# Performance work log

Measured on AMD Instinct MI355X. Metric: run time of the kernel, lower is better.

## Reference

```python
import jax, jax.numpy as jnp
import numpy as np

B, S, K, H = 512, 200, 16, 256
EPS_LN = 1e-12
EPS_COS = 1e-6


def layernorm(x, w, b):
    u = x.mean(-1, keepdims=True)
    s = ((x - u) ** 2).mean(-1, keepdims=True)
    return w * (x - u) / jnp.sqrt(s + EPS_LN) + b


def setup_inputs() -> dict:
    key = jax.random.key(0)
    ks = jax.random.split(key, 10)
    inv_sqrt_h = 1.0 / np.sqrt(H)
    inp = {
        "z": jax.random.normal(ks[0], (B, S, H), dtype=jnp.float32),
        "prototypes": jax.random.normal(ks[1], (K, H), dtype=jnp.float32) * inv_sqrt_h,
        "ln1_w": jnp.ones((H,), jnp.float32), "ln1_b": jnp.zeros((H,), jnp.float32),
        "ln2_w": jnp.ones((H,), jnp.float32), "ln2_b": jnp.zeros((H,), jnp.float32),
        "ln3_w": jnp.ones((H,), jnp.float32), "ln3_b": jnp.zeros((H,), jnp.float32),
        "ln4_w": jnp.ones((H,), jnp.float32), "ln4_b": jnp.zeros((H,), jnp.float32),
        "ln5_w": jnp.ones((H,), jnp.float32), "ln5_b": jnp.zeros((H,), jnp.float32),
        "w_weight": jax.random.normal(ks[2], (H, H), dtype=jnp.float32) * inv_sqrt_h,
        "w_bias": jax.random.normal(ks[3], (H,), dtype=jnp.float32) * 0.02,
        "b_prime": jax.random.normal(ks[4], (H,), dtype=jnp.float32) * 0.02,
        "alphas": jax.random.normal(ks[5], (S, H), dtype=jnp.float32) * 0.02,
        "beta_input_seq": jax.random.normal(ks[6], (K, H), dtype=jnp.float32) * inv_sqrt_h,
        "beta_label_seq": jax.random.normal(ks[7], (K, H), dtype=jnp.float32) * inv_sqrt_h,
        "is_input_seq": 1,
    }
    return inp


def reference(z, prototypes, ln1_w, ln1_b, ln2_w, ln2_b, ln3_w, ln3_b,
              ln4_w, ln4_b, ln5_w, ln5_b, w_weight, w_bias, b_prime,
              alphas, beta_input_seq, beta_label_seq, is_input_seq):
    inv_sqrt_h = 1.0 / np.sqrt(z.shape[-1])

    # ---- intention clustering: cosine-sim of z against each prototype, softmax over K ----
    zn = layernorm(z, ln1_w, ln1_b)                      # [B,S,H]
    pn = layernorm(prototypes, ln2_w, ln2_b)             # [K,H]
    z_norm = jnp.maximum(jnp.linalg.norm(zn, axis=-1), EPS_COS)   # [B,S]
    p_norm = jnp.maximum(jnp.linalg.norm(pn, axis=-1), EPS_COS)   # [K]
    cos = jnp.einsum('bsh,kh->bsk', zn, pn) / (z_norm[..., None] * p_norm[None, None, :])
    p_k_i = jax.nn.softmax(cos * inv_sqrt_h, axis=-1)    # [B,S,K]

    # ---- intention weighting: key transform + bmm attention over positions ----
    keys_tilde = layernorm(z + alphas, ln3_w, ln3_b)                         # [B,S,H]
    keys = keys_tilde + jax.nn.relu(keys_tilde @ w_weight.T + w_bias)        # [B,S,H]
    query = layernorm(b_prime + alphas[-1, :] + z[:, -1, :], ln4_w, ln4_b)   # [B,H]
    scores = jnp.einsum('bsh,bh->bs', keys, query)                           # [B,S]
    p_i = jax.nn.softmax(scores * inv_sqrt_h, axis=-1)                       # [B,S]

    # ---- aggregation ----
    attn = p_k_i * p_i[..., None]                        # [B,S,K]
    beta = beta_input_seq if is_input_seq else beta_label_seq
    enc = beta + jnp.einsum('bsk,bsh->bkh', attn, z)     # [B,K,H]
    return layernorm(enc, ln5_w, ln5_b)
```

## Files before the change

kernel.cpp:

```cpp
#include <hip/hip_runtime.h>
#include <hip/hip_bf16.h>

#define NB 512
#define NS 200
#define NK 16
#define NH 256
#define INV_SQRT_H 0.0625f
#define EPS_LN 1e-12f
#define EPS_COS 1e-6f
#define KTPAD 264

typedef __attribute__((ext_vector_type(8))) short bf16x8;
typedef __attribute__((ext_vector_type(4))) short s16x4;
typedef __attribute__((ext_vector_type(4))) float f32x4;

__device__ __forceinline__ float wred_sum(float v) {
    v += __shfl_xor(v, 1);  v += __shfl_xor(v, 2);  v += __shfl_xor(v, 4);
    v += __shfl_xor(v, 8);  v += __shfl_xor(v, 16); v += __shfl_xor(v, 32);
    return v;
}

__device__ __forceinline__ float red16(float v) {
    v += __shfl_xor(v, 1);  v += __shfl_xor(v, 2);
    v += __shfl_xor(v, 4);  v += __shfl_xor(v, 8);
    return v;
}

__device__ __forceinline__ float red32(float v) {
    v += __shfl_xor(v, 1);  v += __shfl_xor(v, 2);  v += __shfl_xor(v, 4);
    v += __shfl_xor(v, 8);  v += __shfl_xor(v, 16);
    return v;
}

__device__ __forceinline__ float block_sum256(float v, float* scr) {
    v = wred_sum(v);
    int w = threadIdx.x >> 6;
    __syncthreads();
    if ((threadIdx.x & 63) == 0) scr[w] = v;
    __syncthreads();
    return scr[0] + scr[1] + scr[2] + scr[3];
}

__global__ __launch_bounds__(256) void k_prep(
        const float* __restrict__ prot, const float* __restrict__ w2, const float* __restrict__ b2,
        const float* __restrict__ w_weight, __hip_bfloat16* __restrict__ w_bf,
        const float* __restrict__ z, const float* __restrict__ b_prime,
        const float* __restrict__ alphas, const float* __restrict__ w4, const float* __restrict__ b4,
        float* __restrict__ pn_div, float* __restrict__ q) {
    __shared__ float scr[4];
    int t = threadIdx.x;
    int bid = blockIdx.x;
    if (bid == 0) {
        int c = t & 15, k = t >> 4;
        int h0 = c * 4;
        f32x4 x[4];
        float sm = 0.f, sq = 0.f;
#pragma unroll
        for (int j = 0; j < 4; ++j) {
            x[j] = *reinterpret_cast<const f32x4*>(prot + k * NH + h0 + 64 * j);
#pragma unroll
            for (int i = 0; i < 4; ++i) { sm += x[j][i]; sq += x[j][i] * x[j][i]; }
        }
        sm = red16(sm); sq = red16(sq);
        float u = sm * (1.f / NH);
        float var = sq * (1.f / NH) - u * u;
        float rstd = rsqrtf(var + EPS_LN);
        f32x4 pn[4];
        float nsq = 0.f;
#pragma unroll
        for (int j = 0; j < 4; ++j) {
            f32x4 wv = *reinterpret_cast<const f32x4*>(w2 + h0 + 64 * j);
            f32x4 bv = *reinterpret_cast<const f32x4*>(b2 + h0 + 64 * j);
#pragma unroll
            for (int i = 0; i < 4; ++i) {
                pn[j][i] = wv[i] * (x[j][i] - u) * rstd + bv[i];
                nsq += pn[j][i] * pn[j][i];
            }
        }
        nsq = red16(nsq);
        float pinv = 1.f / fmaxf(sqrtf(nsq), EPS_COS);
#pragma unroll
        for (int j = 0; j < 4; ++j) {
            f32x4 o = pn[j] * pinv;
            *reinterpret_cast<f32x4*>(pn_div + k * NH + h0 + 64 * j) = o;
        }
    } else if (bid <= 64) {
        int i = ((bid - 1) * 256 + t) * 4;
        f32x4 w = *reinterpret_cast<const f32x4*>(w_weight + i);
        union { s16x4 v; __hip_bfloat16 h[4]; } u;
#pragma unroll
        for (int j = 0; j < 4; ++j) u.h[j] = __float2bfloat16(w[j]);
        *reinterpret_cast<s16x4*>(w_bf + i) = u.v;
    } else {
        int b = bid - 65;
        float x = b_prime[t] + alphas[(NS - 1) * NH + t] + z[((size_t)b * NS + (NS - 1)) * NH + t];
        float u = block_sum256(x, scr) * (1.f / NH);
        float d = x - u;
        float var = block_sum256(d * d, scr) * (1.f / NH);
        q[b * NH + t] = w4[t] * d * rsqrtf(var + EPS_LN) + b4[t];
    }
}

__global__ __launch_bounds__(256) void k_rows(
        const float* __restrict__ z, const float* __restrict__ pn_div,
        const float* __restrict__ ln1w, const float* __restrict__ ln1b,
        const float* __restrict__ ln3w, const float* __restrict__ ln3b,
        const float* __restrict__ alphas, const float* __restrict__ q,
        float* __restrict__ p_k_i, __hip_bfloat16* __restrict__ kt,
        float* __restrict__ scores) {
    int tid = threadIdx.x;
    int c   = tid & 31;
    int row = blockIdx.x * 8 + (tid >> 5);
    int s   = row % NS;
    int b   = row / NS;
    size_t base = (size_t)row * NH;
    int h0 = c * 8;

    f32x4 zv0 = *reinterpret_cast<const f32x4*>(z + base + h0);
    f32x4 zv1 = *reinterpret_cast<const f32x4*>(z + base + h0 + 4);
    float sm = 0.f, sq = 0.f;
#pragma unroll
    for (int i = 0; i < 4; ++i) { sm += zv0[i] + zv1[i]; sq += zv0[i]*zv0[i] + zv1[i]*zv1[i]; }
    sm = red32(sm); sq = red32(sq);
    float u    = sm * (1.f / NH);
    float var  = sq * (1.f / NH) - u * u;
    float rstd = rsqrtf(var + EPS_LN);

    f32x4 zn0, zn1;
    {
        f32x4 w1a = *reinterpret_cast<const f32x4*>(ln1w + h0);
        f32x4 w1b = *reinterpret_cast<const f32x4*>(ln1w + h0 + 4);
        f32x4 b1a = *reinterpret_cast<const f32x4*>(ln1b + h0);
        f32x4 b1b = *reinterpret_cast<const f32x4*>(ln1b + h0 + 4);
        float nsq = 0.f;
#pragma unroll
        for (int i = 0; i < 4; ++i) {
            zn0[i] = w1a[i] * (zv0[i] - u) * rstd + b1a[i];
            zn1[i] = w1b[i] * (zv1[i] - u) * rstd + b1b[i];
            nsq += zn0[i]*zn0[i] + zn1[i]*zn1[i];
        }
        nsq = red32(nsq);
        float inv_zn = 1.f / fmaxf(sqrtf(nsq), EPS_COS);
        sm = inv_zn;
    }
    float inv_zn = sm;

    float acc[NK];
#pragma unroll
    for (int k = 0; k < NK; ++k) {
        f32x4 pa = *reinterpret_cast<const f32x4*>(pn_div + k * NH + h0);
        f32x4 pb = *reinterpret_cast<const f32x4*>(pn_div + k * NH + h0 + 4);
        acc[k] = zn0[0]*pa[0] + zn0[1]*pa[1] + zn0[2]*pa[2] + zn0[3]*pa[3]
               + zn1[0]*pb[0] + zn1[1]*pb[1] + zn1[2]*pb[2] + zn1[3]*pb[3];
    }
#pragma unroll
    for (int r = 0; r < 4; ++r) {
        int m = 1 << r;
        int n = NK >> r;
        bool hi = (c & m) != 0;
#pragma unroll
        for (int i = 0; i < 8; ++i) {
            if (i < n / 2) {
                float a = acc[2 * i], bb = acc[2 * i + 1];
                float x = hi ? a : bb;
                float y = __shfl_xor(x, m);
                acc[i] = (hi ? bb : a) + y;
            }
        }
    }
    acc[0] += __shfl_xor(acc[0], 16);

    float logit = acc[0] * inv_zn * INV_SQRT_H;
    float mx = logit;
    mx = fmaxf(mx, __shfl_xor(mx, 1)); mx = fmaxf(mx, __shfl_xor(mx, 2));
    mx = fmaxf(mx, __shfl_xor(mx, 4)); mx = fmaxf(mx, __shfl_xor(mx, 8));
    float e = __expf(logit - mx);
    float se = e;
    se += __shfl_xor(se, 1); se += __shfl_xor(se, 2);
    se += __shfl_xor(se, 4); se += __shfl_xor(se, 8);
    if (c < NK) p_k_i[(size_t)row * NK + c] = e / se;

    f32x4 xv0, xv1;
    {
        f32x4 za = *reinterpret_cast<const f32x4*>(z + base + h0);
        f32x4 zb = *reinterpret_cast<const f32x4*>(z + base + h0 + 4);
        f32x4 aa = *reinterpret_cast<const f32x4*>(alphas + s * NH + h0);
        f32x4 ab = *reinterpret_cast<const f32x4*>(alphas + s * NH + h0 + 4);
        xv0 = za + aa; xv1 = zb + ab;
    }
    float sm3 = 0.f, sq3 = 0.f;
#pragma unroll
    for (int i = 0; i < 4; ++i) { sm3 += xv0[i] + xv1[i]; sq3 += xv0[i]*xv0[i] + xv1[i]*xv1[i]; }
    sm3 = red32(sm3); sq3 = red32(sq3);
    float u3 = sm3 * (1.f / NH);
    float v3 = sq3 * (1.f / NH) - u3 * u3;
    float r3 = rsqrtf(v3 + EPS_LN);

    float ktq = 0.f;
    union { bf16x8 v; __hip_bfloat16 h[8]; } kv;
    {
        f32x4 w3a = *reinterpret_cast<const f32x4*>(ln3w + h0);
        f32x4 w3b = *reinterpret_cast<const f32x4*>(ln3w + h0 + 4);
        f32x4 b3a = *reinterpret_cast<const f32x4*>(ln3b + h0);
        f32x4 b3b = *reinterpret_cast<const f32x4*>(ln3b + h0 + 4);
        f32x4 qa  = *reinterpret_cast<const f32x4*>(q + b * NH + h0);
        f32x4 qb  = *reinterpret_cast<const f32x4*>(q + b * NH + h0 + 4);
#pragma unroll
        for (int i = 0; i < 4; ++i) {
            float k0 = w3a[i] * (xv0[i] - u3) * r3 + b3a[i];
            float k1 = w3b[i] * (xv1[i] - u3) * r3 + b3b[i];
            kv.h[i]     = __float2bfloat16(k0);
            kv.h[i + 4] = __float2bfloat16(k1);
            ktq += k0 * qa[i] + k1 * qb[i];
        }
    }
    *reinterpret_cast<bf16x8*>(kt + base + h0) = kv.v;
    ktq = red32(ktq);
    if (c == 0) scores[row] = ktq;
}

__global__ __launch_bounds__(256) void k_gemm_scores(
        const __hip_bfloat16* __restrict__ kt, const __hip_bfloat16* __restrict__ w_bf,
        const float* __restrict__ w_bias, const float* __restrict__ q,
        float* __restrict__ scores) {
    __shared__ __hip_bfloat16 kt_lds[64 * KTPAD];
    __shared__ float sc[4][64];
    int tid = threadIdx.x, wave = tid >> 6, lane = tid & 63;
    int g = lane >> 4, cc = lane & 15;
    int row0 = blockIdx.x * 64;
    int n_base = wave * 64;

#pragma unroll
    for (int u = 0; u < 8; ++u) {
        int ci = u * 256 + tid;
        bf16x8 v = *reinterpret_cast<const bf16x8*>(kt + (size_t)row0 * NH + ci * 8);
        int r = ci >> 5;
        int col = (ci & 31) * 8;
        *reinterpret_cast<bf16x8*>(&kt_lds[r * KTPAD + col]) = v;
    }
    __syncthreads();

    f32x4 acc[4][4];
#pragma unroll
    for (int mf = 0; mf < 4; ++mf)
#pragma unroll
        for (int nf = 0; nf < 4; ++nf) { f32x4 zz = {0.f, 0.f, 0.f, 0.f}; acc[mf][nf] = zz; }

#pragma unroll
    for (int ks = 0; ks < 8; ++ks) {
        bf16x8 a[4], bb[4];
#pragma unroll
        for (int mf = 0; mf < 4; ++mf)
            a[mf] = *reinterpret_cast<const bf16x8*>(&kt_lds[(mf * 16 + cc) * KTPAD + ks * 32 + g * 8]);
#pragma unroll
        for (int nf = 0; nf < 4; ++nf)
            bb[nf] = *reinterpret_cast<const bf16x8*>(
                w_bf + (size_t)(n_base + nf * 16 + cc) * NH + ks * 32 + g * 8);
#pragma unroll
        for (int mf = 0; mf < 4; ++mf)
#pragma unroll
            for (int nf = 0; nf < 4; ++nf)
                acc[mf][nf] = __builtin_amdgcn_mfma_f32_16x16x32_bf16(a[mf], bb[nf], acc[mf][nf], 0, 0, 0);
    }

    int b_lo = row0 / NS, b_hi = (row0 + 63) / NS;
    float q_lo[4], q_hi[4];
#pragma unroll
    for (int nf = 0; nf < 4; ++nf) {
        int n = n_base + nf * 16 + cc;
        q_lo[nf] = q[b_lo * NH + n];
        q_hi[nf] = q[b_hi * NH + n];
    }

#pragma unroll
    for (int mf = 0; mf < 4; ++mf) {
#pragma unroll
        for (int r = 0; r < 4; ++r) {
            int m = mf * 16 + g * 4 + r;
            int row = row0 + m;
            bool hi = (row / NS) != b_lo;
            float partial = 0.f;
#pragma unroll
            for (int nf = 0; nf < 4; ++nf) {
                int n = n_base + nf * 16 + cc;
                float uval = acc[mf][nf][r] + w_bias[n];
                partial += fmaxf(uval, 0.f) * (hi ? q_hi[nf] : q_lo[nf]);
            }
            partial += __shfl_xor(partial, 1, 16);
            partial += __shfl_xor(partial, 2, 16);
            partial += __shfl_xor(partial, 4, 16);
            partial += __shfl_xor(partial, 8, 16);
            if (cc == 0) sc[wave][m] = partial;
        }
    }
    __syncthreads();
    if (tid < 64)
        scores[row0 + tid] += sc[0][tid] + sc[1][tid] + sc[2][tid] + sc[3][tid];
}

__global__ __launch_bounds__(512) void k_final(
        const float* __restrict__ z, const float* __restrict__ scores,
        const float* __restrict__ p_k_i,
        const float* __restrict__ beta_in, const float* __restrict__ beta_lb,
        const int* __restrict__ flag,
        const float* __restrict__ ln5w, const float* __restrict__ ln5b,
        float* __restrict__ out) {
    __shared__ float p_i[NS];
    __shared__ f32x4 attn4[NS * 4];
    __shared__ f32x4 encp[NK][64];
    int tid = threadIdx.x, lane = tid & 63, wave = tid >> 6;
    int b = blockIdx.x;

    if (wave == 0) {
        float l[4]; float mx = -1e30f;
#pragma unroll
        for (int j = 0; j < 4; ++j) {
            int s = lane + 64 * j;
            l[j] = (s < NS) ? scores[b * NS + s] * INV_SQRT_H : -1e30f;
            mx = fmaxf(mx, l[j]);
        }
#pragma unroll
        for (int m = 1; m < 64; m <<= 1) mx = fmaxf(mx, __shfl_xor(mx, m));
        float ev[4]; float se = 0.f;
#pragma unroll
        for (int j = 0; j < 4; ++j) {
            int s = lane + 64 * j;
            ev[j] = (s < NS) ? __expf(l[j] - mx) : 0.f;
            se += ev[j];
        }
        se = wred_sum(se);
        float inv = 1.f / se;
#pragma unroll
        for (int j = 0; j < 4; ++j) {
            int s = lane + 64 * j;
            if (s < NS) p_i[s] = ev[j] * inv;
        }
    }
    __syncthreads();
    for (int idx = tid; idx < NS * 4; idx += 512) {
        f32x4 pk = *reinterpret_cast<const f32x4*>(p_k_i + (size_t)b * NS * NK + idx * 4);
        attn4[idx] = pk * p_i[idx >> 2];
    }
    __syncthreads();

    const float* beta = (*flag) ? beta_in : beta_lb;
    int kg = wave & 3;
    int sh = wave >> 2;
    int k0 = kg * 4;
    int h0 = lane * 4;
    f32x4 acc[4];
#pragma unroll
    for (int kk = 0; kk < 4; ++kk) {
        if (sh == 0)
            acc[kk] = *reinterpret_cast<const f32x4*>(beta + (k0 + kk) * NH + h0);
        else
            { f32x4 zz = {0.f,0.f,0.f,0.f}; acc[kk] = zz; }
    }

    const float* zb = z + (size_t)b * NS * NH + h0;
    int s0 = sh * 100;
    for (int s = s0; s < s0 + 100; s += 4) {
        f32x4 zv0 = *reinterpret_cast<const f32x4*>(zb + (s + 0) * NH);
        f32x4 zv1 = *reinterpret_cast<const f32x4*>(zb + (s + 1) * NH);
        f32x4 zv2 = *reinterpret_cast<const f32x4*>(zb + (s + 2) * NH);
        f32x4 zv3 = *reinterpret_cast<const f32x4*>(zb + (s + 3) * NH);
        f32x4 at0 = attn4[(s + 0) * 4 + kg];
        f32x4 at1 = attn4[(s + 1) * 4 + kg];
        f32x4 at2 = attn4[(s + 2) * 4 + kg];
        f32x4 at3 = attn4[(s + 3) * 4 + kg];
#pragma unroll
        for (int kk = 0; kk < 4; ++kk)
            acc[kk] += at0[kk] * zv0 + at1[kk] * zv1 + at2[kk] * zv2 + at3[kk] * zv3;
    }

    if (sh == 1) {
#pragma unroll
        for (int kk = 0; kk < 4; ++kk) encp[k0 + kk][lane] = acc[kk];
    }
    __syncthreads();
    if (sh == 0) {
        f32x4 w5 = *reinterpret_cast<const f32x4*>(ln5w + h0);
        f32x4 b5 = *reinterpret_cast<const f32x4*>(ln5b + h0);
#pragma unroll
        for (int kk = 0; kk < 4; ++kk) {
            acc[kk] += encp[k0 + kk][lane];
            float sm = acc[kk][0] + acc[kk][1] + acc[kk][2] + acc[kk][3];
            float sq = acc[kk][0]*acc[kk][0] + acc[kk][1]*acc[kk][1]
                     + acc[kk][2]*acc[kk][2] + acc[kk][3]*acc[kk][3];
            sm = wred_sum(sm); sq = wred_sum(sq);
            float u = sm * (1.f / NH);
            float var = sq * (1.f / NH) - u * u;
            float rstd = rsqrtf(var + EPS_LN);
            f32x4 o;
#pragma unroll
            for (int j = 0; j < 4; ++j) o[j] = w5[j] * (acc[kk][j] - u) * rstd + b5[j];
            *reinterpret_cast<f32x4*>(out + ((size_t)b * NK + k0 + kk) * NH + h0) = o;
        }
    }
}

extern "C" void kernel_launch(void* const* d_in, const int* in_sizes, int n_in,
                              void* d_out, int out_size, void* d_ws, size_t ws_size,
                              hipStream_t stream) {
    const float* z        = (const float*)d_in[0];
    const float* prot     = (const float*)d_in[1];
    const float* ln1w     = (const float*)d_in[2];
    const float* ln1b     = (const float*)d_in[3];
    const float* ln2w     = (const float*)d_in[4];
    const float* ln2b     = (const float*)d_in[5];
    const float* ln3w     = (const float*)d_in[6];
    const float* ln3b     = (const float*)d_in[7];
    const float* ln4w     = (const float*)d_in[8];
    const float* ln4b     = (const float*)d_in[9];
    const float* ln5w     = (const float*)d_in[10];
    const float* ln5b     = (const float*)d_in[11];
    const float* w_weight = (const float*)d_in[12];
    const float* w_bias   = (const float*)d_in[13];
    const float* b_prime  = (const float*)d_in[14];
    const float* alphas   = (const float*)d_in[15];
    const float* beta_in  = (const float*)d_in[16];
    const float* beta_lb  = (const float*)d_in[17];
    const int*   flag     = (const int*)d_in[18];
    float* out = (float*)d_out;

    char* ws = (char*)d_ws;
    float*          pn_div = (float*)(ws);
    float*          q      = (float*)(ws + 16384);
    __hip_bfloat16* w_bf   = (__hip_bfloat16*)(ws + 540672);
    float*          p_k_i  = (float*)(ws + 671744);
    float*          scores = (float*)(ws + 7225344);
    __hip_bfloat16* kt     = (__hip_bfloat16*)(ws + 7634944);

    k_prep<<<577, 256, 0, stream>>>(prot, ln2w, ln2b, w_weight, w_bf,
                                    z, b_prime, alphas, ln4w, ln4b, pn_div, q);
    k_rows<<<NB * NS / 8, 256, 0, stream>>>(z, pn_div, ln1w, ln1b, ln3w, ln3b,
                                            alphas, q, p_k_i, kt, scores);
    k_gemm_scores<<<NB * NS / 64, 256, 0, stream>>>(kt, w_bf, w_bias, q, scores);
    k_final<<<NB, 512, 0, stream>>>(z, scores, p_k_i, beta_in, beta_lb, flag, ln5w, ln5b, out);
}
```

Before: 317.0 us.

## Compute cosine logits via bf16 MFMA on raw z with folded LayerNorm constants

The prototype projection is rewritten algebraically: LN1 weight is folded into bf16 prototypes, and per-prototype constants A and B are precomputed so logits become rstd*(z·p̃ - u*A) + B. Each block now handles 64 rows, stages bf16 z in LDS, runs a 16x16x32 MFMA for the z-by-prototype product, and does the softmax over K per row. This removes the per-row shuffle-transpose dot-product reduction. The scores epilogue in the GEMM kernel also replaces per-row shuffle reductions with an LDS transpose-sum. Rounding raw z to bf16 before subtracting the mean can lose precision when rows have a large mean.

```diff
diff --git a/kernel.cpp b/kernel.cpp
--- a/kernel.cpp
+++ b/kernel.cpp
@@ -43,10 +43,12 @@
 
 __global__ __launch_bounds__(256) void k_prep(
         const float* __restrict__ prot, const float* __restrict__ w2, const float* __restrict__ b2,
+        const float* __restrict__ ln1w, const float* __restrict__ ln1b,
         const float* __restrict__ w_weight, __hip_bfloat16* __restrict__ w_bf,
         const float* __restrict__ z, const float* __restrict__ b_prime,
         const float* __restrict__ alphas, const float* __restrict__ w4, const float* __restrict__ b4,
-        float* __restrict__ pn_div, float* __restrict__ q) {
+        __hip_bfloat16* __restrict__ ptil, float* __restrict__ Acst, float* __restrict__ Bcst,
+        float* __restrict__ q) {
     __shared__ float scr[4];
     int t = threadIdx.x;
     int bid = blockIdx.x;
@@ -79,11 +81,23 @@
         }
         nsq = red16(nsq);
         float pinv = 1.f / fmaxf(sqrtf(nsq), EPS_COS);
-#pragma unroll
-        for (int j = 0; j < 4; ++j) {
+        float asum = 0.f, bsum = 0.f;
+#pragma unroll
+        for (int j = 0; j < 4; ++j) {
+            f32x4 w1 = *reinterpret_cast<const f32x4*>(ln1w + h0 + 64 * j);
+            f32x4 b1 = *reinterpret_cast<const f32x4*>(ln1b + h0 + 64 * j);
             f32x4 o = pn[j] * pinv;
-            *reinterpret_cast<f32x4*>(pn_div + k * NH + h0 + 64 * j) = o;
-        }
+            union { s16x4 v; __hip_bfloat16 h[4]; } pt;
+#pragma unroll
+            for (int i = 0; i < 4; ++i) {
+                pt.h[i] = __float2bfloat16(w1[i] * o[i]);
+                asum += w1[i] * o[i];
+                bsum += b1[i] * o[i];
+            }
+            *reinterpret_cast<s16x4*>(ptil + k * NH + h0 + 64 * j) = pt.v;
+        }
+        asum = red16(asum); bsum = red16(bsum);
+        if (c == 0) { Acst[k] = asum; Bcst[k] = bsum; }
     } else if (bid <= 64) {
         int i = ((bid - 1) * 256 + t) * 4;
         f32x4 w = *reinterpret_cast<const f32x4*>(w_weight + i);
@@ -101,122 +115,147 @@
     }
 }
 
-__global__ __launch_bounds__(256) void k_rows(
-        const float* __restrict__ z, const float* __restrict__ pn_div,
+__global__ __launch_bounds__(256) void k_rows_mfma(
+        const float* __restrict__ z,
         const float* __restrict__ ln1w, const float* __restrict__ ln1b,
         const float* __restrict__ ln3w, const float* __restrict__ ln3b,
         const float* __restrict__ alphas, const float* __restrict__ q,
+        const __hip_bfloat16* __restrict__ ptil,
+        const float* __restrict__ Acst, const float* __restrict__ Bcst,
         float* __restrict__ p_k_i, __hip_bfloat16* __restrict__ kt,
         float* __restrict__ scores) {
+    __shared__ __hip_bfloat16 zbf[64 * KTPAD];
+    __shared__ float zp[64 * 17];
+    __shared__ float uu[64], rs[64], izn[64];
+    __shared__ float Al[16], Bl[16];
+
     int tid = threadIdx.x;
     int c   = tid & 31;
-    int row = blockIdx.x * 8 + (tid >> 5);
-    int s   = row % NS;
-    int b   = row / NS;
-    size_t base = (size_t)row * NH;
+    int grp = tid >> 5;
+    int row0 = blockIdx.x * 64;
     int h0 = c * 8;
 
-    f32x4 zv0 = *reinterpret_cast<const f32x4*>(z + base + h0);
-    f32x4 zv1 = *reinterpret_cast<const f32x4*>(z + base + h0 + 4);
-    float sm = 0.f, sq = 0.f;
-#pragma unroll
-    for (int i = 0; i < 4; ++i) { sm += zv0[i] + zv1[i]; sq += zv0[i]*zv0[i] + zv1[i]*zv1[i]; }
-    sm = red32(sm); sq = red32(sq);
-    float u    = sm * (1.f / NH);
-    float var  = sq * (1.f / NH) - u * u;
-    float rstd = rsqrtf(var + EPS_LN);
-
-    f32x4 zn0, zn1;
-    {
-        f32x4 w1a = *reinterpret_cast<const f32x4*>(ln1w + h0);
-        f32x4 w1b = *reinterpret_cast<const f32x4*>(ln1w + h0 + 4);
-        f32x4 b1a = *reinterpret_cast<const f32x4*>(ln1b + h0);
-        f32x4 b1b = *reinterpret_cast<const f32x4*>(ln1b + h0 + 4);
+    if (tid < 16) { Al[tid] = Acst[tid]; Bl[tid] = Bcst[tid]; }
+
+#pragma unroll 1
+    for (int jr = 0; jr < 8; ++jr) {
+        int rl  = grp + 8 * jr;
+        int row = row0 + rl;
+        int s   = row % NS;
+        int b   = row / NS;
+        size_t base = (size_t)row * NH;
+
+        f32x4 zv0 = *reinterpret_cast<const f32x4*>(z + base + h0);
+        f32x4 zv1 = *reinterpret_cast<const f32x4*>(z + base + h0 + 4);
+        float sm = 0.f, sq = 0.f;
+#pragma unroll
+        for (int i = 0; i < 4; ++i) { sm += zv0[i] + zv1[i]; sq += zv0[i]*zv0[i] + zv1[i]*zv1[i]; }
+        sm = red32(sm); sq = red32(sq);
+        float u    = sm * (1.f / NH);
+        float var  = sq * (1.f / NH) - u * u;
+        float rstd = rsqrtf(var + EPS_LN);
+
         float nsq = 0.f;
-#pragma unroll
-        for (int i = 0; i < 4; ++i) {
-            zn0[i] = w1a[i] * (zv0[i] - u) * rstd + b1a[i];
-            zn1[i] = w1b[i] * (zv1[i] - u) * rstd + b1b[i];
-            nsq += zn0[i]*zn0[i] + zn1[i]*zn1[i];
+        {
+            f32x4 w1a = *reinterpret_cast<const f32x4*>(ln1w + h0);
+            f32x4 w1b = *reinterpret_cast<const f32x4*>(ln1w + h0 + 4);
+            f32x4 b1a = *reinterpret_cast<const f32x4*>(ln1b + h0);
+            f32x4 b1b = *reinterpret_cast<const f32x4*>(ln1b + h0 + 4);
+#pragma unroll
+            for (int i = 0; i < 4; ++i) {
+                float a = w1a[i] * (zv0[i] - u) * rstd + b1a[i];
+                float d = w1b[i] * (zv1[i] - u) * rstd + b1b[i];
+                nsq += a * a + d * d;
+            }
         }
         nsq = red32(nsq);
-        float inv_zn = 1.f / fmaxf(sqrtf(nsq), EPS_COS);
-        sm = inv_zn;
-    }
-    float inv_zn = sm;
-
-    float acc[NK];
-#pragma unroll
-    for (int k = 0; k < NK; ++k) {
-        f32x4 pa = *reinterpret_cast<const f32x4*>(pn_div + k * NH + h0);
-        f32x4 pb = *reinterpret_cast<const f32x4*>(pn_div + k * NH + h0 + 4);
-        acc[k] = zn0[0]*pa[0] + zn0[1]*pa[1] + zn0[2]*pa[2] + zn0[3]*pa[3]
-               + zn1[0]*pb[0] + zn1[1]*pb[1] + zn1[2]*pb[2] + zn1[3]*pb[3];
-    }
-#pragma unroll
-    for (int r = 0; r < 4; ++r) {
-        int m = 1 << r;
-        int n = NK >> r;
-        bool hi = (c & m) != 0;
-#pragma unroll
-        for (int i = 0; i < 8; ++i) {
-            if (i < n / 2) {
-                float a = acc[2 * i], bb = acc[2 * i + 1];
-                float x = hi ? a : bb;
-                float y = __shfl_xor(x, m);
-                acc[i] = (hi ? bb : a) + y;
-            }
-        }
-    }
-    acc[0] += __shfl_xor(acc[0], 16);
-
-    float logit = acc[0] * inv_zn * INV_SQRT_H;
-    float mx = logit;
-    mx = fmaxf(mx, __shfl_xor(mx, 1)); mx = fmaxf(mx, __shfl_xor(mx, 2));
-    mx = fmaxf(mx, __shfl_xor(mx, 4)); mx = fmaxf(mx, __shfl_xor(mx, 8));
-    float e = __expf(logit - mx);
-    float se = e;
-    se += __shfl_xor(se, 1); se += __shfl_xor(se, 2);
-    se += __shfl_xor(se, 4); se += __shfl_xor(se, 8);
-    if (c < NK) p_k_i[(size_t)row * NK + c] = e / se;
-
-    f32x4 xv0, xv1;
-    {
-        f32x4 za = *reinterpret_cast<const f32x4*>(z + base + h0);
-        f32x4 zb = *reinterpret_cast<const f32x4*>(z + base + h0 + 4);
-        f32x4 aa = *reinterpret_cast<const f32x4*>(alphas + s * NH + h0);
-        f32x4 ab = *reinterpret_cast<const f32x4*>(alphas + s * NH + h0 + 4);
-        xv0 = za + aa; xv1 = zb + ab;
-    }
-    float sm3 = 0.f, sq3 = 0.f;
-#pragma unroll
-    for (int i = 0; i < 4; ++i) { sm3 += xv0[i] + xv1[i]; sq3 += xv0[i]*xv0[i] + xv1[i]*xv1[i]; }
-    sm3 = red32(sm3); sq3 = red32(sq3);
-    float u3 = sm3 * (1.f / NH);
-    float v3 = sq3 * (1.f / NH) - u3 * u3;
-    float r3 = rsqrtf(v3 + EPS_LN);
-
-    float ktq = 0.f;
-    union { bf16x8 v; __hip_bfloat16 h[8]; } kv;
-    {
-        f32x4 w3a = *reinterpret_cast<const f32x4*>(ln3w + h0);
-        f32x4 w3b = *reinterpret_cast<const f32x4*>(ln3w + h0 + 4);
-        f32x4 b3a = *reinterpret_cast<const f32x4*>(ln3b + h0);
-        f32x4 b3b = *reinterpret_cast<const f32x4*>(ln3b + h0 + 4);
-        f32x4 qa  = *reinterpret_cast<const f32x4*>(q + b * NH + h0);
-        f32x4 qb  = *reinterpret_cast<const f32x4*>(q + b * NH + h0 + 4);
-#pragma unroll
-        for (int i = 0; i < 4; ++i) {
-            float k0 = w3a[i] * (xv0[i] - u3) * r3 + b3a[i];
-            float k1 = w3b[i] * (xv1[i] - u3) * r3 + b3b[i];
-            kv.h[i]     = __float2bfloat16(k0);
-            kv.h[i + 4] = __float2bfloat16(k1);
-            ktq += k0 * qa[i] + k1 * qb[i];
-        }
-    }
-    *reinterpret_cast<bf16x8*>(kt + base + h0) = kv.v;
-    ktq = red32(ktq);
-    if (c == 0) scores[row] = ktq;
+        float izn_v = 1.f / fmaxf(sqrtf(nsq), EPS_COS);
+
+        {
+            union { bf16x8 v; __hip_bfloat16 h[8]; } zc;
+#pragma unroll
+            for (int i = 0; i < 4; ++i) {
+                zc.h[i]     = __float2bfloat16(zv0[i]);
+                zc.h[i + 4] = __float2bfloat16(zv1[i]);
+            }
+            *reinterpret_cast<bf16x8*>(&zbf[rl * KTPAD + h0]) = zc.v;
+        }
+
+        f32x4 xv0, xv1;
+        {
+            f32x4 aa = *reinterpret_cast<const f32x4*>(alphas + s * NH + h0);
+            f32x4 ab = *reinterpret_cast<const f32x4*>(alphas + s * NH + h0 + 4);
+            xv0 = zv0 + aa; xv1 = zv1 + ab;
+        }
+        float sm3 = 0.f, sq3 = 0.f;
+#pragma unroll
+        for (int i = 0; i < 4; ++i) { sm3 += xv0[i] + xv1[i]; sq3 += xv0[i]*xv0[i] + xv1[i]*xv1[i]; }
+        sm3 = red32(sm3); sq3 = red32(sq3);
+        float u3 = sm3 * (1.f / NH);
+        float v3 = sq3 * (1.f / NH) - u3 * u3;
+        float r3 = rsqrtf(v3 + EPS_LN);
+
+        float ktq = 0.f;
+        union { bf16x8 v; __hip_bfloat16 h[8]; } kv;
+        {
+            f32x4 w3a = *reinterpret_cast<const f32x4*>(ln3w + h0);
+            f32x4 w3b = *reinterpret_cast<const f32x4*>(ln3w + h0 + 4);
+            f32x4 b3a = *reinterpret_cast<const f32x4*>(ln3b + h0);
+            f32x4 b3b = *reinterpret_cast<const f32x4*>(ln3b + h0 + 4);
+            f32x4 qa  = *reinterpret_cast<const f32x4*>(q + b * NH + h0);
+            f32x4 qb  = *reinterpret_cast<const f32x4*>(q + b * NH + h0 + 4);
+#pragma unroll
+            for (int i = 0; i < 4; ++i) {
+                float k0 = w3a[i] * (xv0[i] - u3) * r3 + b3a[i];
+                float k1 = w3b[i] * (xv1[i] - u3) * r3 + b3b[i];
+                kv.h[i]     = __float2bfloat16(k0);
+                kv.h[i + 4] = __float2bfloat16(k1);
+                ktq += k0 * qa[i] + k1 * qb[i];
+            }
+        }
+        *reinterpret_cast<bf16x8*>(kt + base + h0) = kv.v;
+        ktq = red32(ktq);
+        if (c == 0) {
+            scores[row] = ktq;
+            uu[rl] = u; rs[rl] = rstd; izn[rl] = izn_v;
+        }
+    }
+    __syncthreads();
+
+    int wave = tid >> 6, lane = tid & 63;
+    int m = lane & 15, g = lane >> 4;
+    f32x4 acc = {0.f, 0.f, 0.f, 0.f};
+#pragma unroll
+    for (int ks = 0; ks < 8; ++ks) {
+        bf16x8 a = *reinterpret_cast<const bf16x8*>(&zbf[(wave * 16 + m) * KTPAD + ks * 32 + g * 8]);
+        bf16x8 bb = *reinterpret_cast<const bf16x8*>(ptil + m * NH + ks * 32 + g * 8);
+        acc = __builtin_amdgcn_mfma_f32_16x16x32_bf16(a, bb, acc, 0, 0, 0);
+    }
+#pragma unroll
+    for (int r = 0; r < 4; ++r)
+        zp[(wave * 16 + g * 4 + r) * 17 + m] = acc[r];
+    __syncthreads();
+
+    if (tid < 64) {
+        float u = uu[tid], rstd = rs[tid], iz = izn[tid];
+        float lg[NK];
+        float mx = -1e30f;
+#pragma unroll
+        for (int k = 0; k < NK; ++k) {
+            lg[k] = (rstd * (zp[tid * 17 + k] - u * Al[k]) + Bl[k]) * iz * INV_SQRT_H;
+            mx = fmaxf(mx, lg[k]);
+        }
+        float se = 0.f;
+#pragma unroll
+        for (int k = 0; k < NK; ++k) { lg[k] = __expf(lg[k] - mx); se += lg[k]; }
+        float inv = 1.f / se;
+        float* dst = p_k_i + (size_t)(row0 + tid) * NK;
+#pragma unroll
+        for (int jj = 0; jj < 4; ++jj) {
+            f32x4 o = { lg[4*jj] * inv, lg[4*jj+1] * inv, lg[4*jj+2] * inv, lg[4*jj+3] * inv };
+            *reinterpret_cast<f32x4*>(dst + 4 * jj) = o;
+        }
+    }
 }
 
 __global__ __launch_bounds__(256) void k_gemm_scores(
@@ -271,28 +310,37 @@
         q_lo[nf] = q[b_lo * NH + n];
         q_hi[nf] = q[b_hi * NH + n];
     }
-
+    float part[4][4];
 #pragma unroll
     for (int mf = 0; mf < 4; ++mf) {
 #pragma unroll
         for (int r = 0; r < 4; ++r) {
-            int m = mf * 16 + g * 4 + r;
-            int row = row0 + m;
+            int row = row0 + mf * 16 + g * 4 + r;
             bool hi = (row / NS) != b_lo;
-            float partial = 0.f;
+            float p = 0.f;
 #pragma unroll
             for (int nf = 0; nf < 4; ++nf) {
                 int n = n_base + nf * 16 + cc;
                 float uval = acc[mf][nf][r] + w_bias[n];
-                partial += fmaxf(uval, 0.f) * (hi ? q_hi[nf] : q_lo[nf]);
-            }
-            partial += __shfl_xor(partial, 1, 16);
-            partial += __shfl_xor(partial, 2, 16);
-            partial += __shfl_xor(partial, 4, 16);
-            partial += __shfl_xor(partial, 8, 16);
-            if (cc == 0) sc[wave][m] = partial;
-        }
-    }
+                p += fmaxf(uval, 0.f) * (hi ? q_hi[nf] : q_lo[nf]);
+            }
+            part[mf][r] = p;
+        }
+    }
+    __syncthreads();
+    float* rp = (float*)kt_lds;
+#pragma unroll
+    for (int mf = 0; mf < 4; ++mf)
+#pragma unroll
+        for (int r = 0; r < 4; ++r)
+            rp[(mf * 16 + g * 4 + r) * 65 + wave * 16 + cc] = part[mf][r];
+    __syncthreads();
+
+    int rr = tid & 63, seg = tid >> 6;
+    float ss = 0.f;
+#pragma unroll
+    for (int j = 0; j < 16; ++j) ss += rp[rr * 65 + seg * 16 + j];
+    sc[seg][rr] = ss;
     __syncthreads();
     if (tid < 64)
         scores[row0 + tid] += sc[0][tid] + sc[1][tid] + sc[2][tid] + sc[3][tid];
@@ -424,17 +472,19 @@
     float* out = (float*)d_out;
 
     char* ws = (char*)d_ws;
-    float*          pn_div = (float*)(ws);
+    __hip_bfloat16* ptil   = (__hip_bfloat16*)(ws);
+    float*          Acst   = (float*)(ws + 8192);
+    float*          Bcst   = (float*)(ws + 8256);
     float*          q      = (float*)(ws + 16384);
     __hip_bfloat16* w_bf   = (__hip_bfloat16*)(ws + 540672);
     float*          p_k_i  = (float*)(ws + 671744);
     float*          scores = (float*)(ws + 7225344);
     __hip_bfloat16* kt     = (__hip_bfloat16*)(ws + 7634944);
 
-    k_prep<<<577, 256, 0, stream>>>(prot, ln2w, ln2b, w_weight, w_bf,
-                                    z, b_prime, alphas, ln4w, ln4b, pn_div, q);
-    k_rows<<<NB * NS / 8, 256, 0, stream>>>(z, pn_div, ln1w, ln1b, ln3w, ln3b,
-                                            alphas, q, p_k_i, kt, scores);
+    k_prep<<<577, 256, 0, stream>>>(prot, ln2w, ln2b, ln1w, ln1b, w_weight, w_bf,
+                                    z, b_prime, alphas, ln4w, ln4b, ptil, Acst, Bcst, q);
+    k_rows_mfma<<<NB * NS / 64, 256, 0, stream>>>(z, ln1w, ln1b, ln3w, ln3b, alphas, q,
+                                                  ptil, Acst, Bcst, p_k_i, kt, scores);
     k_gemm_scores<<<NB * NS / 64, 256, 0, stream>>>(kt, w_bf, w_bias, q, scores);
     k_final<<<NB, 512, 0, stream>>>(z, scores, p_k_i, beta_in, beta_lb, flag, ln5w, ln5b, out);
 }
```

Result: faster. 269.9 us (-14.9%).
